# Optimization experiments

Measured on AMD Instinct MI355X. Metric: run time of the kernel, lower is better.

## Reference

```python
import jax, jax.numpy as jnp
import numpy as np

D_MODEL = 2048
NUM_HEADS = 32
NUM_KV_HEADS = 8
HEAD_DIM = D_MODEL // NUM_HEADS  # 64
KV_DIM = NUM_KV_HEADS * HEAD_DIM  # 512


def setup_inputs() -> dict:
    key = jax.random.key(0)
    ks = jax.random.split(key, 9)
    s = 1.0 / np.sqrt(D_MODEL)
    x = jax.random.normal(ks[0], (4, 1024, D_MODEL), dtype=jnp.float32)
    Wq = jax.random.uniform(ks[1], (D_MODEL, D_MODEL), jnp.float32, -s, s)
    bq = jax.random.uniform(ks[2], (D_MODEL,), jnp.float32, -s, s)
    Wk = jax.random.uniform(ks[3], (D_MODEL, KV_DIM), jnp.float32, -s, s)
    bk = jax.random.uniform(ks[4], (KV_DIM,), jnp.float32, -s, s)
    Wv = jax.random.uniform(ks[5], (D_MODEL, KV_DIM), jnp.float32, -s, s)
    bv = jax.random.uniform(ks[6], (KV_DIM,), jnp.float32, -s, s)
    Wo = jax.random.uniform(ks[7], (D_MODEL, D_MODEL), jnp.float32, -s, s)
    bo = jax.random.uniform(ks[8], (D_MODEL,), jnp.float32, -s, s)
    return {"x": x, "Wq": Wq, "bq": bq, "Wk": Wk, "bk": bk,
            "Wv": Wv, "bv": bv, "Wo": Wo, "bo": bo}


def reference(x, Wq, bq, Wk, bk, Wv, bv, Wo, bo):
    B, S, _ = x.shape
    g = NUM_HEADS // NUM_KV_HEADS  # heads per kv head
    # projections
    q = (x @ Wq + bq).reshape(B, S, NUM_HEADS, HEAD_DIM).transpose(0, 2, 1, 3)   # [B,H,S,d]
    k = (x @ Wk + bk).reshape(B, S, NUM_KV_HEADS, HEAD_DIM).transpose(0, 2, 1, 3)  # [B,Hkv,S,d]
    v = (x @ Wv + bv).reshape(B, S, NUM_KV_HEADS, HEAD_DIM).transpose(0, 2, 1, 3)
    # repeat_interleave KV heads across query-head groups
    k = jnp.repeat(k, g, axis=1)  # [B,H,S,d]
    v = jnp.repeat(v, g, axis=1)
    scores = jnp.einsum('bhqd,bhkd->bhqk', q, k) / np.sqrt(HEAD_DIM)  # [B,H,S,S]
    attn = jax.nn.softmax(scores, axis=-1)
    ctx = jnp.einsum('bhqk,bhkd->bhqd', attn, v)  # [B,H,S,d]
    ctx = ctx.transpose(0, 2, 1, 3).reshape(B, S, D_MODEL)
    return ctx @ Wo + bo
```

## Files before the change

### kernel.cpp

```cpp
#include <hip/hip_runtime.h>
#include <stdint.h>

typedef unsigned short u16;
typedef __attribute__((ext_vector_type(8))) __bf16 bf16x8;
typedef __attribute__((ext_vector_type(4))) __bf16 bf16x4;
typedef __attribute__((ext_vector_type(4))) float f32x4;

#define QSCALE 0.1803368801111204f

#if __has_builtin(__builtin_amdgcn_exp2f)
#define EXP2(x) __builtin_amdgcn_exp2f(x)
#else
#define EXP2(x) exp2f(x)
#endif

__device__ __forceinline__ u16 f2bf(float f) {
  uint32_t u = __float_as_uint(f);
  u += 0x7fffu + ((u >> 16) & 1u);
  return (u16)(u >> 16);
}
__device__ __forceinline__ float bf2f(u16 h) {
  return __uint_as_float(((uint32_t)h) << 16);
}

__device__ __forceinline__ void gl_lds16(const u16* g, u16* l) {
  __builtin_amdgcn_global_load_lds(
      (const __attribute__((address_space(1))) unsigned int*)g,
      (__attribute__((address_space(3))) unsigned int*)l, 16, 0, 0);
}

__global__ void detect_dtype(const u16* __restrict__ x, int* __restrict__ flag) {
  __shared__ int any_huge;
  if (threadIdx.x == 0) any_huge = 0;
  __syncthreads();
  int huge = 0;
  for (int i = threadIdx.x; i < 4096; i += 256) {
    float v = bf2f(x[i]);
    if (!(fabsf(v) < 1e6f)) huge = 1;
  }
  if (huge) any_huge = 1;
  __syncthreads();
  if (threadIdx.x == 0) *flag = any_huge;
}

__global__ __launch_bounds__(256) void prep(
    const void* __restrict__ Wq, const void* __restrict__ Wk,
    const void* __restrict__ Wv, const void* __restrict__ Wo,
    const void* __restrict__ x,
    const void* __restrict__ bq, const void* __restrict__ bk,
    const void* __restrict__ bv, const void* __restrict__ bo,
    u16* __restrict__ WT, u16* __restrict__ WoT, u16* __restrict__ xb,
    float* __restrict__ biasf, const int* __restrict__ flag) {
  __shared__ u16 tile[32][33];
  const int fl = *flag;
  int id = blockIdx.x;
  const int tid = threadIdx.x;
  if (id < 10240) {
    const void* in; u16* out; int N, rowoff;
    if (id < 4096)      { in = Wq; out = WT;  N = 2048; rowoff = 0; }
    else if (id < 5120) { in = Wk; out = WT;  N = 512;  rowoff = 2048; id -= 4096; }
    else if (id < 6144) { in = Wv; out = WT;  N = 512;  rowoff = 2560; id -= 5120; }
    else                { in = Wo; out = WoT; N = 2048; rowoff = 0;    id -= 6144; }
    int tiles_x = N >> 5;
    int nb = (id % tiles_x) * 32, kb = (id / tiles_x) * 32;
    int tx = tid & 31, ty = tid >> 5;
#pragma unroll
    for (int i = 0; i < 32; i += 8) {
      size_t idx = (size_t)(kb + ty + i) * N + nb + tx;
      tile[ty + i][tx] = fl ? f2bf(((const float*)in)[idx]) : ((const u16*)in)[idx];
    }
    __syncthreads();
#pragma unroll
    for (int i = 0; i < 32; i += 8)
      out[(size_t)(rowoff + nb + ty + i) * 2048 + kb + tx] = tile[tx][ty + i];
  } else if (id < 14336) {
    int i = ((id - 10240) * 256 + tid) * 8;
    if (fl) {
      const float* xf = (const float*)x;
      union { u16 o[8]; uint4 v; } u;
#pragma unroll
      for (int j = 0; j < 8; ++j) u.o[j] = f2bf(xf[i + j]);
      *(uint4*)&xb[i] = u.v;
    } else {
      *(uint4*)&xb[i] = *(const uint4*)&((const u16*)x)[i];
    }
  } else {
    int i = (id - 14336) * 256 + tid;
    if (i < 5120) {
      const void* src; int idx;
      if (i < 2048)      { src = bq; idx = i; }
      else if (i < 2560) { src = bk; idx = i - 2048; }
      else if (i < 3072) { src = bv; idx = i - 2560; }
      else               { src = bo; idx = i - 3072; }
      biasf[i] = fl ? ((const float*)src)[idx] : bf2f(((const u16*)src)[idx]);
    }
  }
}

template <int MODE>
__global__ __launch_bounds__(256) void gemm_bt(
    const u16* __restrict__ A, const u16* __restrict__ BT,
    const float* __restrict__ bias,
    u16* __restrict__ o0, u16* __restrict__ o1, u16* __restrict__ o2,
    int N, int K, const int* __restrict__ flag) {
  constexpr int BK = 32;
  __shared__ u16 Al[128 * BK];
  __shared__ u16 Bl[128 * BK];
  const int tid = threadIdx.x;
  const int wave = tid >> 6, lane = tid & 63;
  const int ln = lane & 15, quad = lane >> 4;
  const int m0 = blockIdx.y * 128, n0 = blockIdx.x * 128;
  const int wm = (wave >> 1) * 64, wn = (wave & 1) * 64;
  const int fl = (MODE == 0) ? *flag : 0;

  f32x4 acc[4][4];
#pragma unroll
  for (int i = 0; i < 4; ++i)
#pragma unroll
    for (int j = 0; j < 4; ++j) acc[i][j] = {0.f, 0.f, 0.f, 0.f};

  const int cb = wave * 128 + lane;

  for (int kt = 0; kt < K; kt += BK) {
    __syncthreads();
#pragma unroll
    for (int i = 0; i < 2; ++i) {
      int c = cb + i * 64;
      gl_lds16(&A[(size_t)(m0 + (c >> 2)) * K + kt + (c & 3) * 8], &Al[c * 8]);
    }
#pragma unroll
    for (int i = 0; i < 2; ++i) {
      int c = cb + i * 64;
      gl_lds16(&BT[(size_t)(n0 + (c >> 2)) * K + kt + (c & 3) * 8], &Bl[c * 8]);
    }
    __asm__ volatile("s_waitcnt vmcnt(0)" ::: "memory");
    __syncthreads();
    bf16x8 af[4], bfr[4];
#pragma unroll
    for (int i = 0; i < 4; ++i)
      af[i] = *(const bf16x8*)&Al[(wm + i * 16 + ln) * BK + quad * 8];
#pragma unroll
    for (int j = 0; j < 4; ++j)
      bfr[j] = *(const bf16x8*)&Bl[(wn + j * 16 + ln) * BK + quad * 8];
#pragma unroll
    for (int i = 0; i < 4; ++i)
#pragma unroll
      for (int j = 0; j < 4; ++j)
        acc[i][j] = __builtin_amdgcn_mfma_f32_16x16x32_bf16(af[i], bfr[j], acc[i][j], 0, 0, 0);
  }

#pragma unroll
  for (int j = 0; j < 4; ++j) {
    int gn = n0 + wn + j * 16 + ln;
    float bs = bias[gn];
#pragma unroll
    for (int i = 0; i < 4; ++i) {
      int gmb = m0 + wm + i * 16 + quad * 4;
#pragma unroll
      for (int r = 0; r < 4; ++r) {
        int gm = gmb + r;
        float v = acc[i][j][r] + bs;
        if (MODE == 0) {
          size_t idx = (size_t)gm * N + gn;
          if (fl) ((float*)o0)[idx] = v;
          else o0[idx] = f2bf(v);
        } else {
          int b = gm >> 10, s = gm & 1023;
          if (gn < 2048) {
            v *= QSCALE;
            int h = gn >> 6, dd = gn & 63;
            o0[(((size_t)(b * 32 + h)) * 1024 + s) * 64 + dd] = f2bf(v);
          } else if (gn < 2560) {
            int n2 = gn - 2048, h = n2 >> 6, dd = n2 & 63;
            o1[(((size_t)(b * 8 + h)) * 1024 + s) * 64 + dd] = f2bf(v);
          } else {
            int n2 = gn - 2560, h = n2 >> 6, dd = n2 & 63;
            o2[(((size_t)(b * 8 + h)) * 64 + dd) * 1024 + s] = f2bf(v);
          }
        }
      }
    }
  }
}

__global__ __launch_bounds__(256) void attn_kernel(
    const u16* __restrict__ q_ws, const u16* __restrict__ k_ws,
    const u16* __restrict__ vt_ws, u16* __restrict__ ctx) {
  __shared__ u16 Kl[64 * 72];
  __shared__ u16 Vl[64 * 72];
  __shared__ u16 Pl[4 * 16 * 68];
  const int tid = threadIdx.x;
  const int wave = tid >> 6, lane = tid & 63;
  const int ln = lane & 15, quad = lane >> 4;
  const int qt = blockIdx.x;
  const int bh = blockIdx.y;
  const int b = bh >> 5, h = bh & 31, kvh = h >> 2;
  const int q0 = qt * 64;
  const size_t qbase = (size_t)bh * 1024 * 64;
  const u16* kptr = k_ws + (size_t)(b * 8 + kvh) * 1024 * 64;
  const u16* vptr = vt_ws + (size_t)(b * 8 + kvh) * 64 * 1024;

  const int qrow = q0 + wave * 16 + ln;
  bf16x8 qf0 = *(const bf16x8*)&q_ws[qbase + (size_t)qrow * 64 + quad * 8];
  bf16x8 qf1 = *(const bf16x8*)&q_ws[qbase + (size_t)qrow * 64 + 32 + quad * 8];

  float lsum = 0.f;
  f32x4 oacc[4];
#pragma unroll
  for (int t = 0; t < 4; ++t) oacc[t] = {0.f, 0.f, 0.f, 0.f};

  const int kr0 = tid >> 3, kp0 = (tid & 7) * 8;
  const int kr1 = kr0 + 32;
  const int prow = wave * 16 * 68 + ln * 68;

  uint4 kv0 = *(const uint4*)&kptr[(size_t)kr0 * 64 + kp0];
  uint4 kv1 = *(const uint4*)&kptr[(size_t)kr1 * 64 + kp0];
  uint4 vv0 = *(const uint4*)&vptr[(size_t)kr0 * 1024 + kp0];
  uint4 vv1 = *(const uint4*)&vptr[(size_t)kr1 * 1024 + kp0];

  for (int kb = 0; kb < 1024; kb += 64) {
    __syncthreads();
    *(uint4*)&Kl[kr0 * 72 + kp0] = kv0;
    *(uint4*)&Kl[kr1 * 72 + kp0] = kv1;
    *(uint4*)&Vl[kr0 * 72 + kp0] = vv0;
    *(uint4*)&Vl[kr1 * 72 + kp0] = vv1;
    __syncthreads();

    {
      int nkb = (kb + 64) & 1023;
      kv0 = *(const uint4*)&kptr[(size_t)(nkb + kr0) * 64 + kp0];
      kv1 = *(const uint4*)&kptr[(size_t)(nkb + kr1) * 64 + kp0];
      vv0 = *(const uint4*)&vptr[(size_t)kr0 * 1024 + nkb + kp0];
      vv1 = *(const uint4*)&vptr[(size_t)kr1 * 1024 + nkb + kp0];
    }

    f32x4 sacc[4];
#pragma unroll
    for (int t = 0; t < 4; ++t) sacc[t] = {0.f, 0.f, 0.f, 0.f};
#pragma unroll
    for (int t = 0; t < 4; ++t) {
      bf16x8 kf0 = *(const bf16x8*)&Kl[(t * 16 + ln) * 72 + quad * 8];
      bf16x8 kf1 = *(const bf16x8*)&Kl[(t * 16 + ln) * 72 + 32 + quad * 8];
      sacc[t] = __builtin_amdgcn_mfma_f32_16x16x32_bf16(kf0, qf0, sacc[t], 0, 0, 0);
      sacc[t] = __builtin_amdgcn_mfma_f32_16x16x32_bf16(kf1, qf1, sacc[t], 0, 0, 0);
    }

    uint2 pk[4];
#pragma unroll
    for (int t = 0; t < 4; ++t) {
      float p0 = EXP2(sacc[t][0]);
      float p1 = EXP2(sacc[t][1]);
      float p2 = EXP2(sacc[t][2]);
      float p3 = EXP2(sacc[t][3]);
      lsum += (p0 + p1) + (p2 + p3);
      pk[t].x = __builtin_amdgcn_perm(__float_as_uint(p1), __float_as_uint(p0), 0x07060302u);
      pk[t].y = __builtin_amdgcn_perm(__float_as_uint(p3), __float_as_uint(p2), 0x07060302u);
    }
#pragma unroll
    for (int t = 0; t < 4; ++t)
      *(uint2*)&Pl[prow + t * 16 + quad * 4] = pk[t];
    __asm__ volatile("s_waitcnt lgkmcnt(0)" ::: "memory");

    bf16x8 pf0 = *(const bf16x8*)&Pl[prow + quad * 8];
    bf16x8 pf1 = *(const bf16x8*)&Pl[prow + 32 + quad * 8];

#pragma unroll
    for (int t = 0; t < 4; ++t) {
      bf16x8 vf0 = *(const bf16x8*)&Vl[(t * 16 + ln) * 72 + quad * 8];
      bf16x8 vf1 = *(const bf16x8*)&Vl[(t * 16 + ln) * 72 + 32 + quad * 8];
      oacc[t] = __builtin_amdgcn_mfma_f32_16x16x32_bf16(vf0, pf0, oacc[t], 0, 0, 0);
      oacc[t] = __builtin_amdgcn_mfma_f32_16x16x32_bf16(vf1, pf1, oacc[t], 0, 0, 0);
    }
  }

  float l2 = lsum + __shfl_xor(lsum, 16);
  l2 += __shfl_xor(l2, 32);
  const float inv = 1.0f / l2;

  const size_t obase = (size_t)(b * 1024 + qrow) * 2048 + h * 64;
#pragma unroll
  for (int t = 0; t < 4; ++t) {
    u16 o0 = f2bf(oacc[t][0] * inv);
    u16 o1 = f2bf(oacc[t][1] * inv);
    u16 o2 = f2bf(oacc[t][2] * inv);
    u16 o3 = f2bf(oacc[t][3] * inv);
    uint2 st;
    st.x = (uint32_t)o0 | ((uint32_t)o1 << 16);
    st.y = (uint32_t)o2 | ((uint32_t)o3 << 16);
    *(uint2*)&ctx[obase + t * 16 + quad * 4] = st;
  }
}

extern "C" void kernel_launch(void* const* d_in, const int* in_sizes, int n_in,
                              void* d_out, int out_size, void* d_ws, size_t ws_size,
                              hipStream_t stream) {
  const void* x  = d_in[0];
  const void* Wq = d_in[1];
  const void* bq = d_in[2];
  const void* Wk = d_in[3];
  const void* bk = d_in[4];
  const void* Wv = d_in[5];
  const void* bv = d_in[6];
  const void* Wo = d_in[7];
  const void* bo = d_in[8];
  char* ws = (char*)d_ws;

  u16* WT    = (u16*)(ws + 0);
  u16* WoT   = (u16*)(ws + 12582912);
  u16* q_ws  = (u16*)(ws + 20971520);
  u16* k_ws  = (u16*)(ws + 37748736);
  u16* vt_ws = (u16*)(ws + 41943040);
  u16* c_ws  = (u16*)(ws + 46137344);
  u16* xb    = (u16*)(ws + 62914560);
  float* biasf = (float*)(ws + 79691776);
  int* flag  = (int*)(ws + 79712256);

  detect_dtype<<<1, 256, 0, stream>>>((const u16*)x, flag);
  prep<<<14356, 256, 0, stream>>>(Wq, Wk, Wv, Wo, x, bq, bk, bv, bo,
                                  WT, WoT, xb, biasf, flag);

  gemm_bt<3><<<dim3(24, 32), 256, 0, stream>>>(xb, WT, biasf, q_ws, k_ws, vt_ws,
                                               3072, 2048, flag);
  attn_kernel<<<dim3(16, 128), 256, 0, stream>>>(q_ws, k_ws, vt_ws, c_ws);
  gemm_bt<0><<<dim3(16, 32), 256, 0, stream>>>(c_ws, WoT, biasf + 3072,
                                               (u16*)d_out, nullptr, nullptr,
                                               2048, 2048, flag);
}
```

Baseline: 315.5 us.

## Swizzle GEMM LDS tiles and vectorize epilogue stores via MFMA operand swap

New measurement: 309.4 us. No clear change (-1.9%).

```diff
diff --git a/kernel.cpp b/kernel.cpp
--- a/kernel.cpp
+++ b/kernel.cpp
@@ -21,6 +21,9 @@
 }
 __device__ __forceinline__ float bf2f(u16 h) {
   return __uint_as_float(((uint32_t)h) << 16);
+}
+__device__ __forceinline__ uint32_t pack2bf(float a, float b) {
+  return (uint32_t)f2bf(a) | ((uint32_t)f2bf(b) << 16);
 }
 
 __device__ __forceinline__ void gl_lds16(const u16* g, u16* l) {
@@ -97,21 +100,60 @@
   }
 }
 
-template <int MODE>
-__global__ __launch_bounds__(256) void gemm_bt(
+template <bool SWAP>
+__device__ __forceinline__ void gemm_loop(
+    const u16* __restrict__ A, const u16* __restrict__ BT,
+    u16* __restrict__ Al, u16* __restrict__ Bl,
+    int m0, int n0, int K, int tid, f32x4 acc[4][4]) {
+  const int wave = tid >> 6, lane = tid & 63;
+  const int ln = lane & 15, quad = lane >> 4;
+  const int wm = (wave >> 1) * 64, wn = (wave & 1) * 64;
+  const int sw8 = (quad ^ ((ln >> 1) & 3)) * 8;
+
+  const int c0 = wave * 128 + lane, c1 = c0 + 64;
+  const int kq0 = ((c0 & 3) ^ ((c0 >> 3) & 3)) * 8;
+  const int kq1 = ((c1 & 3) ^ ((c1 >> 3) & 3)) * 8;
+  const u16* a0 = &A[(size_t)(m0 + (c0 >> 2)) * K + kq0];
+  const u16* a1 = &A[(size_t)(m0 + (c1 >> 2)) * K + kq1];
+  const u16* b0 = &BT[(size_t)(n0 + (c0 >> 2)) * K + kq0];
+  const u16* b1 = &BT[(size_t)(n0 + (c1 >> 2)) * K + kq1];
+
+  for (int kt = 0; kt < K; kt += 32) {
+    __syncthreads();
+    gl_lds16(a0 + kt, &Al[c0 * 8]);
+    gl_lds16(a1 + kt, &Al[c1 * 8]);
+    gl_lds16(b0 + kt, &Bl[c0 * 8]);
+    gl_lds16(b1 + kt, &Bl[c1 * 8]);
+    __asm__ volatile("s_waitcnt vmcnt(0)" ::: "memory");
+    __syncthreads();
+    bf16x8 af[4], bfr[4];
+#pragma unroll
+    for (int i = 0; i < 4; ++i)
+      af[i] = *(const bf16x8*)&Al[(wm + i * 16 + ln) * 32 + sw8];
+#pragma unroll
+    for (int j = 0; j < 4; ++j)
+      bfr[j] = *(const bf16x8*)&Bl[(wn + j * 16 + ln) * 32 + sw8];
+#pragma unroll
+    for (int i = 0; i < 4; ++i)
+#pragma unroll
+      for (int j = 0; j < 4; ++j)
+        acc[i][j] = SWAP
+            ? __builtin_amdgcn_mfma_f32_16x16x32_bf16(bfr[j], af[i], acc[i][j], 0, 0, 0)
+            : __builtin_amdgcn_mfma_f32_16x16x32_bf16(af[i], bfr[j], acc[i][j], 0, 0, 0);
+  }
+}
+
+__global__ __launch_bounds__(256) void gemm_qkv(
     const u16* __restrict__ A, const u16* __restrict__ BT,
     const float* __restrict__ bias,
-    u16* __restrict__ o0, u16* __restrict__ o1, u16* __restrict__ o2,
-    int N, int K, const int* __restrict__ flag) {
-  constexpr int BK = 32;
-  __shared__ u16 Al[128 * BK];
-  __shared__ u16 Bl[128 * BK];
+    u16* __restrict__ qo, u16* __restrict__ ko, u16* __restrict__ vo, int K) {
+  __shared__ u16 Al[128 * 32];
+  __shared__ u16 Bl[128 * 32];
   const int tid = threadIdx.x;
   const int wave = tid >> 6, lane = tid & 63;
   const int ln = lane & 15, quad = lane >> 4;
   const int m0 = blockIdx.y * 128, n0 = blockIdx.x * 128;
   const int wm = (wave >> 1) * 64, wn = (wave & 1) * 64;
-  const int fl = (MODE == 0) ? *flag : 0;
 
   f32x4 acc[4][4];
 #pragma unroll
@@ -119,65 +161,84 @@
 #pragma unroll
     for (int j = 0; j < 4; ++j) acc[i][j] = {0.f, 0.f, 0.f, 0.f};
 
-  const int cb = wave * 128 + lane;
-
-  for (int kt = 0; kt < K; kt += BK) {
-    __syncthreads();
-#pragma unroll
-    for (int i = 0; i < 2; ++i) {
-      int c = cb + i * 64;
-      gl_lds16(&A[(size_t)(m0 + (c >> 2)) * K + kt + (c & 3) * 8], &Al[c * 8]);
-    }
-#pragma unroll
-    for (int i = 0; i < 2; ++i) {
-      int c = cb + i * 64;
-      gl_lds16(&BT[(size_t)(n0 + (c >> 2)) * K + kt + (c & 3) * 8], &Bl[c * 8]);
-    }
-    __asm__ volatile("s_waitcnt vmcnt(0)" ::: "memory");
-    __syncthreads();
-    bf16x8 af[4], bfr[4];
-#pragma unroll
-    for (int i = 0; i < 4; ++i)
-      af[i] = *(const bf16x8*)&Al[(wm + i * 16 + ln) * BK + quad * 8];
-#pragma unroll
-    for (int j = 0; j < 4; ++j)
-      bfr[j] = *(const bf16x8*)&Bl[(wn + j * 16 + ln) * BK + quad * 8];
-#pragma unroll
-    for (int i = 0; i < 4; ++i)
-#pragma unroll
-      for (int j = 0; j < 4; ++j)
-        acc[i][j] = __builtin_amdgcn_mfma_f32_16x16x32_bf16(af[i], bfr[j], acc[i][j], 0, 0, 0);
-  }
+  if (blockIdx.x < 20) {
+    gemm_loop<true>(A, BT, Al, Bl, m0, n0, K, tid, acc);
+    const bool isq = (n0 < 2048);
+#pragma unroll
+    for (int j = 0; j < 4; ++j) {
+      int nbase = n0 + wn + j * 16 + quad * 4;
+      float4 bsv = *(const float4*)&bias[nbase];
+      int n2 = isq ? nbase : nbase - 2048;
+      int h = n2 >> 6, dd = n2 & 63;
+      u16* o = isq ? qo : ko;
+      int hmul = isq ? 32 : 8;
+#pragma unroll
+      for (int i = 0; i < 4; ++i) {
+        int m = m0 + wm + i * 16 + ln;
+        int b = m >> 10, s = m & 1023;
+        float v0 = acc[i][j][0] + bsv.x, v1 = acc[i][j][1] + bsv.y;
+        float v2 = acc[i][j][2] + bsv.z, v3 = acc[i][j][3] + bsv.w;
+        if (isq) { v0 *= QSCALE; v1 *= QSCALE; v2 *= QSCALE; v3 *= QSCALE; }
+        uint2 st; st.x = pack2bf(v0, v1); st.y = pack2bf(v2, v3);
+        *(uint2*)&o[(((size_t)(b * hmul + h)) * 1024 + s) * 64 + dd] = st;
+      }
+    }
+  } else {
+    gemm_loop<false>(A, BT, Al, Bl, m0, n0, K, tid, acc);
+#pragma unroll
+    for (int j = 0; j < 4; ++j) {
+      int gn = n0 + wn + j * 16 + ln;
+      float bs = bias[gn];
+      int n2 = gn - 2560, h = n2 >> 6, dd = n2 & 63;
+#pragma unroll
+      for (int i = 0; i < 4; ++i) {
+        int mb = m0 + wm + i * 16 + quad * 4;
+        int b = mb >> 10, sb = mb & 1023;
+        uint2 st;
+        st.x = pack2bf(acc[i][j][0] + bs, acc[i][j][1] + bs);
+        st.y = pack2bf(acc[i][j][2] + bs, acc[i][j][3] + bs);
+        *(uint2*)&vo[(((size_t)(b * 8 + h)) * 64 + dd) * 1024 + sb] = st;
+      }
+    }
+  }
+}
+
+__global__ __launch_bounds__(256) void gemm_o(
+    const u16* __restrict__ A, const u16* __restrict__ BT,
+    const float* __restrict__ bias, u16* __restrict__ o0,
+    int N, int K, const int* __restrict__ flag) {
+  __shared__ u16 Al[128 * 32];
+  __shared__ u16 Bl[128 * 32];
+  const int tid = threadIdx.x;
+  const int wave = tid >> 6, lane = tid & 63;
+  const int ln = lane & 15, quad = lane >> 4;
+  const int m0 = blockIdx.y * 128, n0 = blockIdx.x * 128;
+  const int wm = (wave >> 1) * 64, wn = (wave & 1) * 64;
+  const int fl = *flag;
+
+  f32x4 acc[4][4];
+#pragma unroll
+  for (int i = 0; i < 4; ++i)
+#pragma unroll
+    for (int j = 0; j < 4; ++j) acc[i][j] = {0.f, 0.f, 0.f, 0.f};
+
+  gemm_loop<true>(A, BT, Al, Bl, m0, n0, K, tid, acc);
 
 #pragma unroll
   for (int j = 0; j < 4; ++j) {
-    int gn = n0 + wn + j * 16 + ln;
-    float bs = bias[gn];
+    int nbase = n0 + wn + j * 16 + quad * 4;
+    float4 bsv = *(const float4*)&bias[nbase];
 #pragma unroll
     for (int i = 0; i < 4; ++i) {
-      int gmb = m0 + wm + i * 16 + quad * 4;
-#pragma unroll
-      for (int r = 0; r < 4; ++r) {
-        int gm = gmb + r;
-        float v = acc[i][j][r] + bs;
-        if (MODE == 0) {
-          size_t idx = (size_t)gm * N + gn;
-          if (fl) ((float*)o0)[idx] = v;
-          else o0[idx] = f2bf(v);
-        } else {
-          int b = gm >> 10, s = gm & 1023;
-          if (gn < 2048) {
-            v *= QSCALE;
-            int h = gn >> 6, dd = gn & 63;
-            o0[(((size_t)(b * 32 + h)) * 1024 + s) * 64 + dd] = f2bf(v);
-          } else if (gn < 2560) {
-            int n2 = gn - 2048, h = n2 >> 6, dd = n2 & 63;
-            o1[(((size_t)(b * 8 + h)) * 1024 + s) * 64 + dd] = f2bf(v);
-          } else {
-            int n2 = gn - 2560, h = n2 >> 6, dd = n2 & 63;
-            o2[(((size_t)(b * 8 + h)) * 64 + dd) * 1024 + s] = f2bf(v);
-          }
-        }
+      int m = m0 + wm + i * 16 + ln;
+      float v0 = acc[i][j][0] + bsv.x, v1 = acc[i][j][1] + bsv.y;
+      float v2 = acc[i][j][2] + bsv.z, v3 = acc[i][j][3] + bsv.w;
+      if (fl) {
+        float4 st = {v0, v1, v2, v3};
+        *(float4*)&((float*)o0)[(size_t)m * N + nbase] = st;
+      } else {
+        uint2 st; st.x = pack2bf(v0, v1); st.y = pack2bf(v2, v3);
+        *(uint2*)&o0[(size_t)m * N + nbase] = st;
       }
     }
   }
@@ -280,13 +341,9 @@
   const size_t obase = (size_t)(b * 1024 + qrow) * 2048 + h * 64;
 #pragma unroll
   for (int t = 0; t < 4; ++t) {
-    u16 o0 = f2bf(oacc[t][0] * inv);
-    u16 o1 = f2bf(oacc[t][1] * inv);
-    u16 o2 = f2bf(oacc[t][2] * inv);
-    u16 o3 = f2bf(oacc[t][3] * inv);
     uint2 st;
-    st.x = (uint32_t)o0 | ((uint32_t)o1 << 16);
-    st.y = (uint32_t)o2 | ((uint32_t)o3 << 16);
+    st.x = pack2bf(oacc[t][0] * inv, oacc[t][1] * inv);
+    st.y = pack2bf(oacc[t][2] * inv, oacc[t][3] * inv);
     *(uint2*)&ctx[obase + t * 16 + quad * 4] = st;
   }
 }
@@ -319,10 +376,8 @@
   prep<<<14356, 256, 0, stream>>>(Wq, Wk, Wv, Wo, x, bq, bk, bv, bo,
                                   WT, WoT, xb, biasf, flag);
 
-  gemm_bt<3><<<dim3(24, 32), 256, 0, stream>>>(xb, WT, biasf, q_ws, k_ws, vt_ws,
-                                               3072, 2048, flag);
+  gemm_qkv<<<dim3(24, 32), 256, 0, stream>>>(xb, WT, biasf, q_ws, k_ws, vt_ws, 2048);
   attn_kernel<<<dim3(16, 128), 256, 0, stream>>>(q_ws, k_ws, vt_ws, c_ws);
-  gemm_bt<0><<<dim3(16, 32), 256, 0, stream>>>(c_ws, WoT, biasf + 3072,
-                                               (u16*)d_out, nullptr, nullptr,
-                                               2048, 2048, flag);
-}
+  gemm_o<<<dim3(16, 32), 256, 0, stream>>>(c_ws, WoT, biasf + 3072,
+                                           (u16*)d_out, 2048, 2048, flag);
+}
```
